# Optimization experiments

Measured on AMD Instinct MI355X. Metric: run time of the kernel, lower is better.

Reference implementation:

```python
import jax, jax.numpy as jnp
import numpy as np

N, D, L, K = 250000, 16, 6, 64
COST_GAMMA = 0.1
MIN_ZERO_GAMMA = 0.1
EPS = 1e-7  # clip for arccos numerical stability


def setup_inputs() -> dict:
    key = jax.random.key(0)
    k1, k2, k3, k4 = jax.random.split(key, 4)
    xs = jax.random.normal(k1, (N, D), jnp.float32)
    xs = xs / jnp.linalg.norm(xs, axis=1, keepdims=True)  # points on sphere S^{D-1}
    mus = jax.random.normal(k2, (L, D, K), jnp.float32)    # per-layer component locations
    alphas = jax.random.uniform(k3, (L, K), jnp.float32, minval=-1.0, maxval=1.0)
    ws = jax.random.uniform(k4, (L,), jnp.float32, minval=0.0, maxval=1.0)
    return {"xs": xs, "mus": mus, "alphas": alphas, "ws": ws}


def reference(xs, mus, alphas, ws):
    # projx: normalize each mu column onto the sphere (norm over D axis)
    mu_n = mus / jnp.linalg.norm(mus, axis=1, keepdims=True)          # [L, D, K]
    # sphere cost: 0.5 * geodesic_dist^2 = 0.5 * arccos(<x, mu>)^2
    inner = jnp.einsum('nd,ldk->lnk', xs, mu_n)                        # [L, N, K]
    dist = jnp.arccos(jnp.clip(inner, -1.0 + EPS, 1.0 - EPS))
    costs = 0.5 * dist * dist + alphas[:, None, :]                     # [L, N, K]
    # soft-min over components (note sign convention follows original: +gamma*LSE(-c/gamma))
    mincosts = COST_GAMMA * jax.nn.logsumexp(-costs / COST_GAMMA, axis=2)  # [L, N]
    wv = jnp.exp(-ws ** 2)                                             # [L]
    F = jnp.zeros((xs.shape[0],), xs.dtype)
    for i in range(L):  # small fixed layer recurrence
        F = wv[i] * jax.nn.relu(F) + (1.0 - wv[i]) * mincosts[i]
    # smooth min(F, 0): gamma * LSE(-[F,0]/gamma)
    Fz = jnp.stack((F, jnp.zeros_like(F)), axis=-1)
    F = MIN_ZERO_GAMMA * jax.nn.logsumexp(-Fz / MIN_ZERO_GAMMA, axis=-1)
    return F
```

## Files before the change

### kernel.cpp

```cpp
#include <hip/hip_runtime.h>
#include <math.h>

#define NPOINTS 250000
#define LL 6
#define DD 16
#define KK 64
#define TPB 384
#define PTS_PER_BLOCK 128
#define NTILES (PTS_PER_BLOCK / 16)

#define SMC_OFF (PTS_PER_BLOCK * 80)
#define LDS_BYTES (SMC_OFF + LL * PTS_PER_BLOCK * 4)

#define WS_MU 0
#define WS_AV 24576
#define WS_WV 26112

typedef __attribute__((ext_vector_type(8))) short bf16x8;
typedef __attribute__((ext_vector_type(4))) float f32x4;
typedef __attribute__((ext_vector_type(2))) float f32x2;

#if __has_builtin(__builtin_amdgcn_exp2f)
#define EXP2F(x) __builtin_amdgcn_exp2f(x)
#else
#define EXP2F(x) exp2f(x)
#endif
#if __has_builtin(__builtin_amdgcn_logf)
#define LOG2F(x) __builtin_amdgcn_logf(x)
#else
#define LOG2F(x) log2f(x)
#endif

#define C_AA   (-14.426950408889634f)
#define C_GLN2 (0.06931471805599453f)

#define W0  17.797117f
#define VT0 (-45.300328f)
#define VT1 (-28.559404f)
#define VT2 (-27.844414f)
#define VT3 (-30.475230f)
#define VT4 (-36.246253f)
#define VT5 (-27.207285f)

__device__ __forceinline__ f32x2 s2(float v) { f32x2 r; r.x = v; r.y = v; return r; }

__device__ __forceinline__ ushort bf16_rne(float f) {
  unsigned u = __float_as_uint(f);
  unsigned r = u + 0x7FFFu + ((u >> 16) & 1u);
  return (ushort)(r >> 16);
}

__device__ __forceinline__ f32x2 term2(f32x2 xp, f32x2 aaw) {
  f32x2 x2  = xp * xp;
  f32x2 p01 = __builtin_elementwise_fma(s2(VT1), xp, s2(VT0));
  f32x2 p23 = __builtin_elementwise_fma(s2(VT3), xp, s2(VT2));
  f32x2 p45 = __builtin_elementwise_fma(s2(VT5), xp, s2(VT4));
  f32x2 qq  = __builtin_elementwise_fma(x2, p45, p23);
  f32x2 V   = __builtin_elementwise_fma(x2, qq, p01);
  f32x2 t2  = __builtin_elementwise_fma(xp, V, aaw);
  f32x2 e; e.x = EXP2F(t2.x); e.y = EXP2F(t2.y);
  return e;
}

__global__ __launch_bounds__(384) void
prep_kernel(const float* __restrict__ mus,
            const float* __restrict__ alphas,
            const float* __restrict__ wsv,
            char* __restrict__ ws) {
  const int t = threadIdx.x;
  const float* colp = mus + (t >> 6) * (DD * KK) + (t & 63);
  float v[DD];
  float ss = 0.0f;
#pragma unroll
  for (int d = 0; d < DD; ++d) { v[d] = colp[d * KK]; ss = fmaf(v[d], v[d], ss); }
  float inv = -0.5f / sqrtf(ss);
  unsigned hw[8], lw[8];
#pragma unroll
  for (int i = 0; i < 8; ++i) {
    float a0 = v[2 * i] * inv;
    float a1 = v[2 * i + 1] * inv;
    ushort h0 = bf16_rne(a0), h1 = bf16_rne(a1);
    float hf0 = __uint_as_float((unsigned)h0 << 16);
    float hf1 = __uint_as_float((unsigned)h1 << 16);
    ushort l0 = bf16_rne(a0 - hf0), l1 = bf16_rne(a1 - hf1);
    hw[i] = (unsigned)h0 | ((unsigned)h1 << 16);
    lw[i] = (unsigned)l0 | ((unsigned)l1 << 16);
  }
  uint4* colq = (uint4*)(ws + WS_MU + t * 64);
  colq[0] = make_uint4(hw[0], hw[1], hw[2], hw[3]);
  colq[1] = make_uint4(hw[4], hw[5], hw[6], hw[7]);
  colq[2] = make_uint4(lw[0], lw[1], lw[2], lw[3]);
  colq[3] = make_uint4(lw[4], lw[5], lw[6], lw[7]);
  ((float*)(ws + WS_AV))[t] = fmaf(C_AA, alphas[t], -W0);
  if (t < LL) { float x = wsv[t]; ((float*)(ws + WS_WV))[t] = expf(-x * x); }
}

__global__ __launch_bounds__(TPB, 4) void
multiinf_kernel(const float* __restrict__ xs,
                const char* __restrict__ ws,
                float* __restrict__ out) {
  __shared__ __align__(16) char smem[LDS_BYTES];
  float* smc = (float*)(smem + SMC_OFF);
  char* sxu = smem;

  const int tid = threadIdx.x;
  const int w = tid >> 6;
  const int lane = tid & 63;
  const int c = lane & 15;
  const int q = lane >> 4;
  const int h = q & 1;
  const int pbase = blockIdx.x * PTS_PER_BLOCK;

  bf16x8 Am[4];
  f32x2 aaL[4], aaH[4];
#pragma unroll
  for (int cb = 0; cb < 4; ++cb) {
    Am[cb] = *(const bf16x8*)(ws + WS_MU + (w * 64 + cb * 16 + c) * 64 + q * 16);
    f32x4 a4 = *(const f32x4*)(ws + WS_AV + (w * 64 + cb * 16 + q * 4) * 4);
    aaL[cb].x = a4.x; aaL[cb].y = a4.y;
    aaH[cb].x = a4.z; aaH[cb].y = a4.w;
  }

  if (tid < PTS_PER_BLOCK) {
    int gidx = pbase + tid;
    float xv[DD];
    if (gidx < NPOINTS) {
      const float4* x4 = (const float4*)(xs + (size_t)gidx * DD);
#pragma unroll
      for (int j = 0; j < 4; ++j) {
        float4 a = x4[j];
        xv[j * 4 + 0] = a.x; xv[j * 4 + 1] = a.y;
        xv[j * 4 + 2] = a.z; xv[j * 4 + 3] = a.w;
      }
    } else {
#pragma unroll
      for (int d = 0; d < DD; ++d) xv[d] = 0.0f;
    }
    unsigned hw[8], lw[8];
#pragma unroll
    for (int i = 0; i < 8; ++i) {
      ushort h0 = bf16_rne(xv[2 * i]);
      ushort h1 = bf16_rne(xv[2 * i + 1]);
      float hf0 = __uint_as_float((unsigned)h0 << 16);
      float hf1 = __uint_as_float((unsigned)h1 << 16);
      ushort l0 = bf16_rne(xv[2 * i] - hf0);
      ushort l1 = bf16_rne(xv[2 * i + 1] - hf1);
      hw[i] = (unsigned)h0 | ((unsigned)h1 << 16);
      lw[i] = (unsigned)l0 | ((unsigned)l1 << 16);
    }
    uint4* pq = (uint4*)(sxu + tid * 80);
    pq[0] = make_uint4(hw[0], hw[1], hw[2], hw[3]);
    pq[1] = make_uint4(hw[4], hw[5], hw[6], hw[7]);
    pq[2] = make_uint4(lw[0], lw[1], lw[2], lw[3]);
    pq[3] = make_uint4(lw[4], lw[5], lw[6], lw[7]);
  }

  __syncthreads();

  float* smcw = smc + w * PTS_PER_BLOCK;
  const char* bbase = sxu + c * 80 + h * 16;
  const f32x4 zero4 = {0.0f, 0.0f, 0.0f, 0.0f};
#pragma unroll
  for (int t = 0; t < NTILES; ++t) {
    bf16x8 Bh = *(const bf16x8*)(bbase + t * 1280);
    bf16x8 Bl = *(const bf16x8*)(bbase + t * 1280 + 32);
    f32x2 S01 = s2(0.0f), S23 = s2(0.0f);
#pragma unroll
    for (int cb = 0; cb < 4; ++cb) {
      f32x4 acc = __builtin_amdgcn_mfma_f32_16x16x32_bf16(Am[cb], Bh, zero4, 0, 0, 0);
      acc = __builtin_amdgcn_mfma_f32_16x16x32_bf16(Am[cb], Bl, acc, 0, 0, 0);
      f32x2 a01; a01.x = acc[0]; a01.y = acc[1];
      f32x2 a23; a23.x = acc[2]; a23.y = acc[3];
      S01 += term2(a01, aaL[cb]);
      S23 += term2(a23, aaH[cb]);
    }
    f32x2 Sf = S01 + S23;
    float St = Sf.x + Sf.y;
    St += __shfl_xor(St, 16, 64);
    St += __shfl_xor(St, 32, 64);
    if (lane < 16) smcw[t * 16 + c] = St;
  }
  __syncthreads();

  if (tid < PTS_PER_BLOCK) {
    const float* swv = (const float*)(ws + WS_WV);
    float F = 0.0f;
#pragma unroll
    for (int l = 0; l < LL; ++l) {
      float wv = swv[l];
      float mc = C_GLN2 * LOG2F(smc[l * PTS_PER_BLOCK + tid]);
      F = fmaf(wv, fmaxf(F, 0.0f), (1.0f - wv) * mc);
    }
    int idx = pbase + tid;
    if (idx < NPOINTS) {
      float e = EXP2F(F * C_AA);
      out[idx] = C_GLN2 * LOG2F(1.0f + e);
    }
  }
}

extern "C" void kernel_launch(void* const* d_in, const int* in_sizes, int n_in,
                              void* d_out, int out_size, void* d_ws, size_t ws_size,
                              hipStream_t stream) {
  const float* xs = (const float*)d_in[0];
  const float* mus = (const float*)d_in[1];
  const float* alphas = (const float*)d_in[2];
  const float* wsv = (const float*)d_in[3];
  float* out = (float*)d_out;
  char* ws = (char*)d_ws;
  (void)ws_size;

  prep_kernel<<<1, 384, 0, stream>>>(mus, alphas, wsv, ws);
  const int blocks = (NPOINTS + PTS_PER_BLOCK - 1) / PTS_PER_BLOCK;
  multiinf_kernel<<<blocks, TPB, 0, stream>>>(xs, ws, out);
}
```

Baseline: 100.8 us.

## Give each wave its own 16 points across all layers, dropping block syncs

Work is re-partitioned so each wave owns 16 points and loops over all 6 layers, instead of each wave owning one layer for 128 points. This removes both __syncthreads, the cross-wave LDS reduction buffer and the serial tail that ran on only 128 threads. The layer recurrence now stays in registers. In exchange, each wave reloads the mu and alpha fragments for every layer from global or L2 memory, so per-point MFMA reuse of A falls. Blocks also become smaller and more numerous (64 points each).

Measured after the change: 102.1 us. Within noise of the previous version (+1.4%).

```diff
diff --git a/kernel.cpp b/kernel.cpp
--- a/kernel.cpp
+++ b/kernel.cpp
@@ -5,12 +5,13 @@
 #define LL 6
 #define DD 16
 #define KK 64
-#define TPB 384
-#define PTS_PER_BLOCK 128
-#define NTILES (PTS_PER_BLOCK / 16)
 
-#define SMC_OFF (PTS_PER_BLOCK * 80)
-#define LDS_BYTES (SMC_OFF + LL * PTS_PER_BLOCK * 4)
+#define TPB 256
+#define WAVES_PER_BLOCK (TPB / 64)
+#define PTS_PER_WAVE 16
+#define PTS_PER_BLOCK (WAVES_PER_BLOCK * PTS_PER_WAVE)
+
+#define LDS_BYTES (WAVES_PER_BLOCK * PTS_PER_WAVE * 80)
 
 #define WS_MU 0
 #define WS_AV 24576
@@ -100,70 +101,55 @@
                 const char* __restrict__ ws,
                 float* __restrict__ out) {
   __shared__ __align__(16) char smem[LDS_BYTES];
-  float* smc = (float*)(smem + SMC_OFF);
-  char* sxu = smem;
 
   const int tid = threadIdx.x;
-  const int w = tid >> 6;
+  const int wid = tid >> 6;
   const int lane = tid & 63;
   const int c = lane & 15;
   const int q = lane >> 4;
   const int h = q & 1;
-  const int pbase = blockIdx.x * PTS_PER_BLOCK;
+  const int pt0 = blockIdx.x * PTS_PER_BLOCK + wid * PTS_PER_WAVE;
+  char* sx = smem + wid * (PTS_PER_WAVE * 80);
 
-  bf16x8 Am[4];
-  f32x2 aaL[4], aaH[4];
-#pragma unroll
-  for (int cb = 0; cb < 4; ++cb) {
-    Am[cb] = *(const bf16x8*)(ws + WS_MU + (w * 64 + cb * 16 + c) * 64 + q * 16);
-    f32x4 a4 = *(const f32x4*)(ws + WS_AV + (w * 64 + cb * 16 + q * 4) * 4);
-    aaL[cb].x = a4.x; aaL[cb].y = a4.y;
-    aaH[cb].x = a4.z; aaH[cb].y = a4.w;
+  {
+    int gidx = pt0 + c;
+    float4 a = make_float4(0.0f, 0.0f, 0.0f, 0.0f);
+    if (gidx < NPOINTS) a = ((const float4*)(xs + (size_t)gidx * DD))[q];
+    ushort h0 = bf16_rne(a.x), h1 = bf16_rne(a.y);
+    ushort h2 = bf16_rne(a.z), h3 = bf16_rne(a.w);
+    float hf0 = __uint_as_float((unsigned)h0 << 16);
+    float hf1 = __uint_as_float((unsigned)h1 << 16);
+    float hf2 = __uint_as_float((unsigned)h2 << 16);
+    float hf3 = __uint_as_float((unsigned)h3 << 16);
+    ushort l0 = bf16_rne(a.x - hf0), l1 = bf16_rne(a.y - hf1);
+    ushort l2 = bf16_rne(a.z - hf2), l3 = bf16_rne(a.w - hf3);
+    uint2 hwv, lwv;
+    hwv.x = (unsigned)h0 | ((unsigned)h1 << 16);
+    hwv.y = (unsigned)h2 | ((unsigned)h3 << 16);
+    lwv.x = (unsigned)l0 | ((unsigned)l1 << 16);
+    lwv.y = (unsigned)l2 | ((unsigned)l3 << 16);
+    *(uint2*)(sx + c * 80 + q * 8) = hwv;
+    *(uint2*)(sx + c * 80 + 32 + q * 8) = lwv;
   }
 
-  if (tid < PTS_PER_BLOCK) {
-    int gidx = pbase + tid;
-    float xv[DD];
-    if (gidx < NPOINTS) {
-      const float4* x4 = (const float4*)(xs + (size_t)gidx * DD);
+  bf16x8 Bh = *(const bf16x8*)(sx + c * 80 + h * 16);
+  bf16x8 Bl = *(const bf16x8*)(sx + c * 80 + 32 + h * 16);
+
+  const float* swv = (const float*)(ws + WS_WV);
+  const f32x4 zero4 = {0.0f, 0.0f, 0.0f, 0.0f};
+  float F = 0.0f;
+
+#pragma unroll 2
+  for (int l = 0; l < LL; ++l) {
+    bf16x8 Am[4];
+    f32x2 aaL[4], aaH[4];
 #pragma unroll
-      for (int j = 0; j < 4; ++j) {
-        float4 a = x4[j];
-        xv[j * 4 + 0] = a.x; xv[j * 4 + 1] = a.y;
-        xv[j * 4 + 2] = a.z; xv[j * 4 + 3] = a.w;
-      }
-    } else {
-#pragma unroll
-      for (int d = 0; d < DD; ++d) xv[d] = 0.0f;
+    for (int cb = 0; cb < 4; ++cb) {
+      Am[cb] = *(const bf16x8*)(ws + WS_MU + (l * 64 + cb * 16 + c) * 64 + q * 16);
+      f32x4 a4 = *(const f32x4*)(ws + WS_AV + (l * 64 + cb * 16 + q * 4) * 4);
+      aaL[cb].x = a4.x; aaL[cb].y = a4.y;
+      aaH[cb].x = a4.z; aaH[cb].y = a4.w;
     }
-    unsigned hw[8], lw[8];
-#pragma unroll
-    for (int i = 0; i < 8; ++i) {
-      ushort h0 = bf16_rne(xv[2 * i]);
-      ushort h1 = bf16_rne(xv[2 * i + 1]);
-      float hf0 = __uint_as_float((unsigned)h0 << 16);
-      float hf1 = __uint_as_float((unsigned)h1 << 16);
-      ushort l0 = bf16_rne(xv[2 * i] - hf0);
-      ushort l1 = bf16_rne(xv[2 * i + 1] - hf1);
-      hw[i] = (unsigned)h0 | ((unsigned)h1 << 16);
-      lw[i] = (unsigned)l0 | ((unsigned)l1 << 16);
-    }
-    uint4* pq = (uint4*)(sxu + tid * 80);
-    pq[0] = make_uint4(hw[0], hw[1], hw[2], hw[3]);
-    pq[1] = make_uint4(hw[4], hw[5], hw[6], hw[7]);
-    pq[2] = make_uint4(lw[0], lw[1], lw[2], lw[3]);
-    pq[3] = make_uint4(lw[4], lw[5], lw[6], lw[7]);
-  }
-
-  __syncthreads();
-
-  float* smcw = smc + w * PTS_PER_BLOCK;
-  const char* bbase = sxu + c * 80 + h * 16;
-  const f32x4 zero4 = {0.0f, 0.0f, 0.0f, 0.0f};
-#pragma unroll
-  for (int t = 0; t < NTILES; ++t) {
-    bf16x8 Bh = *(const bf16x8*)(bbase + t * 1280);
-    bf16x8 Bl = *(const bf16x8*)(bbase + t * 1280 + 32);
     f32x2 S01 = s2(0.0f), S23 = s2(0.0f);
 #pragma unroll
     for (int cb = 0; cb < 4; ++cb) {
@@ -178,20 +164,13 @@
     float St = Sf.x + Sf.y;
     St += __shfl_xor(St, 16, 64);
     St += __shfl_xor(St, 32, 64);
-    if (lane < 16) smcw[t * 16 + c] = St;
+    float wvl = swv[l];
+    float mc = C_GLN2 * LOG2F(St);
+    F = fmaf(wvl, fmaxf(F, 0.0f), (1.0f - wvl) * mc);
   }
-  __syncthreads();
 
-  if (tid < PTS_PER_BLOCK) {
-    const float* swv = (const float*)(ws + WS_WV);
-    float F = 0.0f;
-#pragma unroll
-    for (int l = 0; l < LL; ++l) {
-      float wv = swv[l];
-      float mc = C_GLN2 * LOG2F(smc[l * PTS_PER_BLOCK + tid]);
-      F = fmaf(wv, fmaxf(F, 0.0f), (1.0f - wv) * mc);
-    }
-    int idx = pbase + tid;
+  if (lane < 16) {
+    int idx = pt0 + c;
     if (idx < NPOINTS) {
       float e = EXP2F(F * C_AA);
       out[idx] = C_GLN2 * LOG2F(1.0f + e);
```
